# Performance work log

Hardware: AMD Instinct MI355X
Metric: run time of the kernel (lower is better)

Reference implementation:

```python
import jax, jax.numpy as jnp
import numpy as np


def setup_inputs() -> dict:
    key = jax.random.key(0)
    k1, k2 = jax.random.split(key)
    N1, N2 = 16384, 16384
    pos1 = jax.random.normal(k1, (N1, 2), dtype=jnp.float32)
    pos2 = jax.random.normal(k2, (N2, 2), dtype=jnp.float32)
    return {"pos1": pos1, "pos2": pos2}


def reference(pos1, pos2):
    # pos1: [N1, 2], pos2: [N2, 2]
    diff = pos1[:, None, :] - pos2[None, :, :]          # [N1, N2, 2]
    dist = jnp.sqrt(jnp.sum(diff * diff, axis=2))       # [N1, N2]
    nearest = jnp.min(dist, axis=1)                     # [N1]
    return jnp.mean(nearest)
```

## Files before the change

### kernel.cpp

```cpp
#include <hip/hip_runtime.h>
#include <math.h>

#define N1 16384
#define N2 16384
#define BLOCK 256
#define PTS 8
#define I_BLOCKS (N1 / (BLOCK * PTS))
#define SLICES 128

__device__ __forceinline__ unsigned int f2key(float f) {
    unsigned int b = __float_as_uint(f);
    return (b & 0x80000000u) ? ~b : (b | 0x80000000u);
}
__device__ __forceinline__ float key2f(unsigned int k) {
    unsigned int b = (k & 0x80000000u) ? (k & 0x7FFFFFFFu) : ~k;
    return __uint_as_float(b);
}

__global__ __launch_bounds__(BLOCK, 4)
void nn_partial(const float2* __restrict__ pos1,
                const float4* __restrict__ pos2,
                unsigned int* __restrict__ keys,
                unsigned int* __restrict__ ticket,
                int slice_f4) {
    const int ib = blockIdx.x;
    const int sl = blockIdx.y;
    const int t  = threadIdx.x;

    if (ib == 0 && sl == 0 && t == 0) *ticket = 0;

    const float4* __restrict__ q = pos2 + (size_t)sl * slice_f4;
    const int i0 = ib * (BLOCK * PTS) + t;

    float x[PTS], y[PTS], m[PTS];
#pragma unroll
    for (int k = 0; k < PTS; ++k) {
        float2 p = pos1[i0 + k * BLOCK];
        x[k] = p.x; y[k] = p.y; m[k] = 3.4e38f;
    }

#pragma unroll 4
    for (int j = 0; j < slice_f4; ++j) {
        float4 qq = q[j];
        float ax = -2.f * qq.x, ay = -2.f * qq.y;
        float az = fmaf(qq.x, qq.x, qq.y * qq.y);
        float bx = -2.f * qq.z, by = -2.f * qq.w;
        float bz = fmaf(qq.z, qq.z, qq.w * qq.w);
#pragma unroll
        for (int k = 0; k < PTS; ++k) {
            m[k] = fminf(m[k], fmaf(x[k], ax, fmaf(y[k], ay, az)));
            m[k] = fminf(m[k], fmaf(x[k], bx, fmaf(y[k], by, bz)));
        }
    }

#pragma unroll
    for (int k = 0; k < PTS; ++k) {
        atomicMin(&keys[i0 + k * BLOCK], f2key(m[k]));
    }
}

__global__ __launch_bounds__(BLOCK)
void nn_finish(const unsigned int* __restrict__ keys,
               const float2* __restrict__ pos1,
               float* __restrict__ blocksums,
               unsigned int* __restrict__ ticket,
               float* __restrict__ out) {
    const int t = threadIdx.x;
    const int i = blockIdx.x * BLOCK + t;

    float g = key2f(keys[i]);
    float2 p = pos1[i];
    float d2 = fmaxf(fmaf(p.x, p.x, p.y * p.y) + g, 0.f);
    float sum = sqrtf(d2);

    for (int off = 32; off > 0; off >>= 1) {
        sum += __shfl_down(sum, off, 64);
    }
    __shared__ float wsum[BLOCK / 64];
    __shared__ int lastflag;
    if ((t & 63) == 0) wsum[t >> 6] = sum;
    __syncthreads();
    if (t == 0) {
        float s = 0.f;
        for (int w = 0; w < BLOCK / 64; ++w) s += wsum[w];
        blocksums[blockIdx.x] = s;
        __threadfence();
        unsigned int old = atomicAdd(ticket, 1u);
        lastflag = (old == gridDim.x - 1) ? 1 : 0;
    }
    __syncthreads();
    if (lastflag && t < 64) {
        volatile float* vb = (volatile float*)blocksums;
        float v = vb[t];
        for (int off = 32; off > 0; off >>= 1) {
            v += __shfl_down(v, off, 64);
        }
        if (t == 0) out[0] = v / (float)N1;
    }
}

extern "C" void kernel_launch(void* const* d_in, const int* in_sizes, int n_in,
                              void* d_out, int out_size, void* d_ws, size_t ws_size,
                              hipStream_t stream) {
    const float2* pos1 = (const float2*)d_in[0];
    const float4* pos2 = (const float4*)d_in[1];
    float* out = (float*)d_out;

    unsigned int* keys = (unsigned int*)d_ws;
    float* blocksums   = (float*)(keys + N1);
    unsigned int* ticket = (unsigned int*)(blocksums + 64);

    const int slice_f4 = (N2 / SLICES) / 2;

    hipMemsetAsync(keys, 0xFF, (size_t)N1 * sizeof(unsigned int), stream);

    dim3 grid1(I_BLOCKS, SLICES);
    nn_partial<<<grid1, BLOCK, 0, stream>>>(pos1, pos2, keys, ticket, slice_f4);
    nn_finish<<<N1 / BLOCK, BLOCK, 0, stream>>>(keys, pos1, blocksums, ticket, out);
}
```

Baseline: 78.12 us.

## Fuse finish into main kernel, broadcast queries via readlane, use packed FMA

Merges the partial nearest-neighbor kernel and the finish kernel into one launch. The last block, found with a ticket counter that the memset starts at 0xFFFFFFFF (hence the GRID-2 check), does the final reduction over all keys. Query points are now loaded once per wave as one point per lane and broadcast with readlane, so they become scalar operands and no longer need per-iteration vector loads. The distance math uses 2-wide vector FMAs so the compiler can emit packed FP32 instructions, and pos1 is pre-scaled by -2. The final sum is now done serially by one block over 16K points, which adds a tail to the critical path.

```diff
diff --git a/kernel.cpp b/kernel.cpp
--- a/kernel.cpp
+++ b/kernel.cpp
@@ -6,96 +6,112 @@
 #define BLOCK 256
 #define PTS 8
 #define I_BLOCKS (N1 / (BLOCK * PTS))
-#define SLICES 128
+#define QG 256
+#define SGROUPS (N2 / QG)
+#define GRID (I_BLOCKS * SGROUPS)
+#define NCHUNK (QG / 64)
 
-__device__ __forceinline__ unsigned int f2key(float f) {
+typedef float v2f __attribute__((ext_vector_type(2)));
+
+static __device__ __forceinline__ unsigned int f2key(float f) {
     unsigned int b = __float_as_uint(f);
     return (b & 0x80000000u) ? ~b : (b | 0x80000000u);
 }
-__device__ __forceinline__ float key2f(unsigned int k) {
+static __device__ __forceinline__ float key2f(unsigned int k) {
     unsigned int b = (k & 0x80000000u) ? (k & 0x7FFFFFFFu) : ~k;
     return __uint_as_float(b);
 }
 
-__global__ __launch_bounds__(BLOCK, 4)
-void nn_partial(const float2* __restrict__ pos1,
-                const float4* __restrict__ pos2,
-                unsigned int* __restrict__ keys,
-                unsigned int* __restrict__ ticket,
-                int slice_f4) {
-    const int ib = blockIdx.x;
-    const int sl = blockIdx.y;
-    const int t  = threadIdx.x;
+__global__ __launch_bounds__(BLOCK, 2)
+void nn_fused(const float2* __restrict__ pos1,
+              const float2* __restrict__ pos2,
+              unsigned int* __restrict__ keys,
+              unsigned int* __restrict__ ticket,
+              float* __restrict__ out) {
+    const int ib   = blockIdx.x & (I_BLOCKS - 1);
+    const int sg   = blockIdx.x / I_BLOCKS;
+    const int t    = threadIdx.x;
+    const int lane = t & 63;
 
-    if (ib == 0 && sl == 0 && t == 0) *ticket = 0;
-
-    const float4* __restrict__ q = pos2 + (size_t)sl * slice_f4;
     const int i0 = ib * (BLOCK * PTS) + t;
-
-    float x[PTS], y[PTS], m[PTS];
+    float xs[PTS], ys[PTS], m[PTS];
 #pragma unroll
     for (int k = 0; k < PTS; ++k) {
         float2 p = pos1[i0 + k * BLOCK];
-        x[k] = p.x; y[k] = p.y; m[k] = 3.4e38f;
+        xs[k] = -2.f * p.x;
+        ys[k] = -2.f * p.y;
+        m[k]  = 3.4e38f;
+    }
+    const float2* qb = pos2 + sg * QG;
+    int qxc, qyc;
+    {
+        float2 q = qb[lane];
+        qxc = __float_as_int(q.x);
+        qyc = __float_as_int(q.y);
     }
 
-#pragma unroll 4
-    for (int j = 0; j < slice_f4; ++j) {
-        float4 qq = q[j];
-        float ax = -2.f * qq.x, ay = -2.f * qq.y;
-        float az = fmaf(qq.x, qq.x, qq.y * qq.y);
-        float bx = -2.f * qq.z, by = -2.f * qq.w;
-        float bz = fmaf(qq.z, qq.z, qq.w * qq.w);
+    for (int c = 0; c < NCHUNK; ++c) {
+        const int cn = (c + 1 < NCHUNK) ? c + 1 : c;
+        float2 qn = qb[cn * 64 + lane];
+        int qxn = __float_as_int(qn.x), qyn = __float_as_int(qn.y);
+
 #pragma unroll
-        for (int k = 0; k < PTS; ++k) {
-            m[k] = fminf(m[k], fmaf(x[k], ax, fmaf(y[k], ay, az)));
-            m[k] = fminf(m[k], fmaf(x[k], bx, fmaf(y[k], by, bz)));
+        for (int j = 0; j < 64; j += 2) {
+            v2f ax, ay;
+            ax.x = __int_as_float(__builtin_amdgcn_readlane(qxc, j));
+            ay.x = __int_as_float(__builtin_amdgcn_readlane(qyc, j));
+            ax.y = __int_as_float(__builtin_amdgcn_readlane(qxc, j + 1));
+            ay.y = __int_as_float(__builtin_amdgcn_readlane(qyc, j + 1));
+            v2f az = __builtin_elementwise_fma(ax, ax, ay * ay);
+#pragma unroll
+            for (int k = 0; k < PTS; ++k) {
+                v2f xk = (v2f){xs[k], xs[k]};
+                v2f yk = (v2f){ys[k], ys[k]};
+                v2f g = __builtin_elementwise_fma(
+                            xk, ax, __builtin_elementwise_fma(yk, ay, az));
+                m[k] = fminf(m[k], fminf(g.x, g.y));
+            }
         }
+        qxc = qxn; qyc = qyn;
     }
 
 #pragma unroll
     for (int k = 0; k < PTS; ++k) {
         atomicMin(&keys[i0 + k * BLOCK], f2key(m[k]));
     }
-}
 
-__global__ __launch_bounds__(BLOCK)
-void nn_finish(const unsigned int* __restrict__ keys,
-               const float2* __restrict__ pos1,
-               float* __restrict__ blocksums,
-               unsigned int* __restrict__ ticket,
-               float* __restrict__ out) {
-    const int t = threadIdx.x;
-    const int i = blockIdx.x * BLOCK + t;
+    __shared__ int lastflag;
+    __threadfence();
+    __syncthreads();
+    if (t == 0) {
+        unsigned int old = __hip_atomic_fetch_add(
+            ticket, 1u, __ATOMIC_ACQ_REL, __HIP_MEMORY_SCOPE_AGENT);
+        lastflag = (old == (unsigned)(GRID - 2));
+    }
+    __syncthreads();
+    if (!lastflag) return;
+    __threadfence();
 
-    float g = key2f(keys[i]);
-    float2 p = pos1[i];
-    float d2 = fmaxf(fmaf(p.x, p.x, p.y * p.y) + g, 0.f);
-    float sum = sqrtf(d2);
-
+    float sum = 0.f;
+#pragma unroll 4
+    for (int r = 0; r < N1 / BLOCK; ++r) {
+        const int i = r * BLOCK + t;
+        unsigned int kk = __hip_atomic_load(&keys[i], __ATOMIC_RELAXED,
+                                            __HIP_MEMORY_SCOPE_AGENT);
+        float g = key2f(kk);
+        float2 p = pos1[i];
+        sum += sqrtf(fmaxf(fmaf(p.x, p.x, p.y * p.y) + g, 0.f));
+    }
     for (int off = 32; off > 0; off >>= 1) {
         sum += __shfl_down(sum, off, 64);
     }
-    __shared__ float wsum[BLOCK / 64];
-    __shared__ int lastflag;
-    if ((t & 63) == 0) wsum[t >> 6] = sum;
+    __shared__ float ws4[BLOCK / 64];
+    if ((t & 63) == 0) ws4[t >> 6] = sum;
     __syncthreads();
     if (t == 0) {
         float s = 0.f;
-        for (int w = 0; w < BLOCK / 64; ++w) s += wsum[w];
-        blocksums[blockIdx.x] = s;
-        __threadfence();
-        unsigned int old = atomicAdd(ticket, 1u);
-        lastflag = (old == gridDim.x - 1) ? 1 : 0;
-    }
-    __syncthreads();
-    if (lastflag && t < 64) {
-        volatile float* vb = (volatile float*)blocksums;
-        float v = vb[t];
-        for (int off = 32; off > 0; off >>= 1) {
-            v += __shfl_down(v, off, 64);
-        }
-        if (t == 0) out[0] = v / (float)N1;
+        for (int w = 0; w < BLOCK / 64; ++w) s += ws4[w];
+        out[0] = s / (float)N1;
     }
 }
 
@@ -103,18 +119,13 @@
                               void* d_out, int out_size, void* d_ws, size_t ws_size,
                               hipStream_t stream) {
     const float2* pos1 = (const float2*)d_in[0];
-    const float4* pos2 = (const float4*)d_in[1];
+    const float2* pos2 = (const float2*)d_in[1];
     float* out = (float*)d_out;
 
-    unsigned int* keys = (unsigned int*)d_ws;
-    float* blocksums   = (float*)(keys + N1);
-    unsigned int* ticket = (unsigned int*)(blocksums + 64);
+    unsigned int* keys   = (unsigned int*)d_ws;
+    unsigned int* ticket = keys + N1;
 
-    const int slice_f4 = (N2 / SLICES) / 2;
+    hipMemsetAsync(keys, 0xFF, (size_t)(N1 + 1) * sizeof(unsigned int), stream);
 
-    hipMemsetAsync(keys, 0xFF, (size_t)N1 * sizeof(unsigned int), stream);
-
-    dim3 grid1(I_BLOCKS, SLICES);
-    nn_partial<<<grid1, BLOCK, 0, stream>>>(pos1, pos2, keys, ticket, slice_f4);
-    nn_finish<<<N1 / BLOCK, BLOCK, 0, stream>>>(keys, pos1, blocksums, ticket, out);
+    nn_fused<<<GRID, BLOCK, 0, stream>>>(pos1, pos2, keys, ticket, out);
 }
```

After: 118.6 us. 1.52x slower.
